# Optimization experiments

Hardware: AMD Instinct MI355X
Metric: run time of the kernel (lower is better)

The kernel has to match this reference:

```python
import jax, jax.numpy as jnp
import numpy as np
from math import ceil, log2

N_ROWS, M_COLS = 4096, 4096
LEVELS, FILT_LEN = 8, 16


def circ_conv(a, b, n):
    # circular convolution of each row of a with filter b, both zero-padded/truncated to length n
    return jnp.fft.irfft(jnp.fft.rfft(a, n=n) * jnp.fft.rfft(b, n=n), n=n)


def forward_level(x, w):
    # one forward DWT step over rows of x using wavelet filter w
    part = x.shape[1] // 2
    g = jnp.flip(w).at[1::2].multiply(-1.0)  # scaling filter g_k = (-1)^k h_{M-k-1}
    we, wo = w[::2], w[1::2]
    ge, go = g[::2], g[1::2]
    even, odd = x[:, ::2], x[:, 1::2]
    details = circ_conv(even, we, part) + circ_conv(odd, wo, part)
    approx = circ_conv(even, ge, part) + circ_conv(odd, go, part)
    return details, approx


def backward_level(details, approx, w):
    # one inverse DWT step: zero-upsample then circular-convolve with synthesis filters
    ws = jnp.flip(w)                       # wavelet synthesis
    ss = w.at[1::2].multiply(-1.0)         # scaling synthesis
    n, md = details.shape
    fd = jnp.zeros((n, 2 * md), details.dtype).at[:, ::2].set(details)
    fa = jnp.zeros((n, 2 * approx.shape[1]), approx.dtype).at[:, ::2].set(approx)
    return circ_conv(fd, ws, 2 * md) + circ_conv(fa, ss, 2 * approx.shape[1])


def despawn(x, wavelet):
    input_length = x.shape[1]
    target = 2 ** ceil(log2(input_length))
    x = jnp.pad(x, ((0, 0), (0, target - input_length)), mode='edge')  # ReplicationPad1d
    levels = wavelet.shape[0]
    approx = x
    coeffs = []
    for lvl in range(levels):
        d, approx = forward_level(approx, wavelet[lvl])
        coeffs.append(d)
    coeffs.append(approx)
    # inverse transform (note: original applies no thresholding in forward)
    rec = coeffs[-1]
    for lvl in reversed(range(levels)):
        rec = backward_level(coeffs[lvl], rec, wavelet[lvl])
    return rec[:, :input_length], jnp.concatenate(coeffs, axis=-1)


def setup_inputs() -> dict:
    key = jax.random.key(0)
    k1, k2 = jax.random.split(key)
    inp = jax.random.normal(k1, (N_ROWS, M_COLS), dtype=jnp.float32)
    wavelet = jax.random.normal(k2, (LEVELS, FILT_LEN), dtype=jnp.float32) * 0.3
    return {"input": inp, "wavelet": wavelet}


def reference(input, wavelet):
    return despawn(input, wavelet)
```

## Files before the change

kernel.cpp:

```cpp
#include <hip/hip_runtime.h>

#define NROWS 4096
#define NCOLS 4096
#define TPB   256


#define LD4(arr, base, vec) { float4 _v = (vec); (arr)[(base)] = _v.x; (arr)[(base)+1] = _v.y; (arr)[(base)+2] = _v.z; (arr)[(base)+3] = _v.w; }
#define LD2(arr, base, vec) { float2 _v = (vec); (arr)[(base)] = _v.x; (arr)[(base)+1] = _v.y; }

__device__ __forceinline__ void fwd_pt(const float* e8, const float* o8,
                                       const float* wl, float& dd, float& aa)
{
    float d = 0.f, a = 0.f;
    #pragma unroll
    for (int t = 0; t < 8; ++t) {
        float e = e8[-t], o = o8[-t];
        d = fmaf(wl[2*t],     e, d);
        d = fmaf(wl[2*t+1],   o, d);
        a = fmaf(wl[15-2*t],  e, a);
        a = fmaf(-wl[14-2*t], o, a);
    }
    dd = d; aa = a;
}

__device__ __forceinline__ void fwd_pt2(const float* e8, const float* o8,
                                        const float* wl, float& dd, float& aa)
{
    float d = 0.f, a = 0.f;
    #pragma unroll
    for (int t = 0; t < 8; ++t) {
        float e = e8[-2*t], o = o8[-2*t];
        d = fmaf(wl[2*t],     e, d);
        d = fmaf(wl[2*t+1],   o, d);
        a = fmaf(wl[15-2*t],  e, a);
        a = fmaf(-wl[14-2*t], o, a);
    }
    dd = d; aa = a;
}

__device__ __forceinline__ void bwd_pt(const float* d8, const float* a8,
                                       const float* wl, float& rr0, float& rr1)
{
    float x = 0.f, y = 0.f;
    #pragma unroll
    for (int t = 0; t < 8; ++t) {
        float dv = d8[-t], av = a8[-t];
        x = fmaf(wl[15-2*t], dv, x);
        x = fmaf(wl[2*t],    av, x);
        y = fmaf(wl[14-2*t], dv, y);
        y = fmaf(-wl[2*t+1], av, y);
    }
    rr0 = x; rr1 = y;
}

__global__ __launch_bounds__(TPB, 5) void despawn_kernel(
    const float* __restrict__ in, const float* __restrict__ wv,
    float* __restrict__ out_rec, float* __restrict__ out_coef)
{
    __shared__ float P0[2048];
    __shared__ float P1[1024];
    __shared__ float Csm[512];
    __shared__ float D0[2048];
    __shared__ float D1[1024];
    __shared__ float D2[512];

    const int tid = threadIdx.x;
    const int row = blockIdx.x;
    const float* rowIn = in + (size_t)row * NCOLS;
    float* crow = out_coef + (size_t)row * NCOLS;
    float* rrow = out_rec  + (size_t)row * NCOLS;

    float wl[16];

    {
        #pragma unroll
        for (int q = 0; q < 16; ++q) wl[q] = wv[q];
        const float4* X4 = (const float4*)rowIn;
        float xw[32];
        #pragma unroll
        for (int j = 0; j < 8; ++j) LD4(xw, 4*j, X4[(4*tid - 4 + j) & 1023]);
        float d[8], a[8];
        #pragma unroll
        for (int p = 0; p < 8; ++p) fwd_pt2(&xw[16 + 2*p], &xw[17 + 2*p], wl, d[p], a[p]);
        const int k0 = tid * 8;
        float4 d0v = make_float4(d[0], d[1], d[2], d[3]);
        float4 d1v = make_float4(d[4], d[5], d[6], d[7]);
        ((float4*)(crow + k0))[0] = d0v;
        ((float4*)(crow + k0))[1] = d1v;
        ((float4*)(D0 + k0))[0]   = d0v;
        ((float4*)(D0 + k0))[1]   = d1v;
        *(float4*)(P0 + (k0 >> 1))        = make_float4(a[0], a[2], a[4], a[6]);
        *(float4*)(P0 + 1024 + (k0 >> 1)) = make_float4(a[1], a[3], a[5], a[7]);
    }
    __syncthreads();

    {
        #pragma unroll
        for (int q = 0; q < 16; ++q) wl[q] = wv[16 + q];
        const float4* E4 = (const float4*)P0;
        const float4* O4 = (const float4*)(P0 + 1024);
        float xe[12], xo[12];
        #pragma unroll
        for (int j = 0; j < 3; ++j) {
            int idx = (tid - 2 + j) & 255;
            LD4(xe, 4*j, E4[idx]); LD4(xo, 4*j, O4[idx]);
        }
        float d[4], a[4];
        #pragma unroll
        for (int p = 0; p < 4; ++p) fwd_pt(&xe[8 + p], &xo[8 + p], wl, d[p], a[p]);
        const int k0 = tid * 4;
        float4 dv = make_float4(d[0], d[1], d[2], d[3]);
        *(float4*)(crow + 2048 + k0) = dv;
        *(float4*)(D1 + k0)          = dv;
        *(float2*)(P1 + (k0 >> 1))       = make_float2(a[0], a[2]);
        *(float2*)(P1 + 512 + (k0 >> 1)) = make_float2(a[1], a[3]);
    }
    __syncthreads();

    {
        #pragma unroll
        for (int q = 0; q < 16; ++q) wl[q] = wv[32 + q];
        const float2* Ev = (const float2*)P1;
        const float2* Ov = (const float2*)(P1 + 512);
        float xe[10], xo[10];
        #pragma unroll
        for (int j = 0; j < 5; ++j) {
            int idx = (tid - 4 + j) & 255;
            LD2(xe, 2*j, Ev[idx]); LD2(xo, 2*j, Ov[idx]);
        }
        float d[2], a[2];
        #pragma unroll
        for (int p = 0; p < 2; ++p) fwd_pt(&xe[8 + p], &xo[8 + p], wl, d[p], a[p]);
        const int k0 = tid * 2;
        float2 dv = make_float2(d[0], d[1]);
        *(float2*)(crow + 3072 + k0) = dv;
        *(float2*)(D2 + k0)          = dv;
        P0[tid]       = a[0];
        P0[256 + tid] = a[1];
    }
    __syncthreads();

    {
        const float* Ein = P0;
        float* aout = P0 + 512;
        int part = 256, cs = 0, cg = 3584;
        for (int lvl = 3; lvl < 8; ++lvl) {
            #pragma unroll
            for (int q = 0; q < 16; ++q) wl[q] = wv[16*lvl + q];
            const int nth = part >> 2;
            if (tid < nth) {
                const int pm = nth - 1;
                const float4* E4 = (const float4*)Ein;
                const float4* O4 = (const float4*)(Ein + part);
                float xe[12], xo[12];
                #pragma unroll
                for (int j = 0; j < 3; ++j) {
                    int idx = (tid - 2 + j) & pm;
                    LD4(xe, 4*j, E4[idx]); LD4(xo, 4*j, O4[idx]);
                }
                float d[4], a[4];
                #pragma unroll
                for (int p = 0; p < 4; ++p) fwd_pt(&xe[8 + p], &xo[8 + p], wl, d[p], a[p]);
                const int k0 = tid * 4;
                float4 dv = make_float4(d[0], d[1], d[2], d[3]);
                *(float4*)(Csm + cs + k0)  = dv;
                *(float4*)(crow + cg + k0) = dv;
                if (lvl == 7) {
                    float4 av = make_float4(a[0], a[1], a[2], a[3]);
                    *(float4*)(Csm + 496 + k0)   = av;
                    *(float4*)(crow + 4080 + k0) = av;
                } else {
                    *(float2*)(aout + (k0 >> 1))               = make_float2(a[0], a[2]);
                    *(float2*)(aout + (part >> 1) + (k0 >> 1)) = make_float2(a[1], a[3]);
                }
            }
            __syncthreads();
            Ein = aout; aout += part; cs += part; cg += part; part >>= 1;
        }
    }

    const float* A = Csm + 496;
    {
        float* outp = P0 + 1024;
        int md = 16, dOff = 480;
        for (int lvl = 7; lvl >= 3; --lvl) {
            #pragma unroll
            for (int q = 0; q < 16; ++q) wl[q] = wv[16*lvl + q];
            const int nth = md >> 2;
            if (tid < nth) {
                const int pm = nth - 1;
                const float4* D4 = (const float4*)(Csm + dOff);
                const float4* A4 = (const float4*)A;
                float xd[12], xa[12];
                #pragma unroll
                for (int j = 0; j < 3; ++j) {
                    int idx = (tid - 2 + j) & pm;
                    LD4(xd, 4*j, D4[idx]); LD4(xa, 4*j, A4[idx]);
                }
                float r0[4], r1[4];
                #pragma unroll
                for (int p = 0; p < 4; ++p) bwd_pt(&xd[8 + p], &xa[8 + p], wl, r0[p], r1[p]);
                const int j0 = tid * 4;
                ((float4*)(outp + 2*j0))[0] = make_float4(r0[0], r1[0], r0[1], r1[1]);
                ((float4*)(outp + 2*j0))[1] = make_float4(r0[2], r1[2], r0[3], r1[3]);
            }
            __syncthreads();
            A = outp; outp += 2*md; md <<= 1; dOff -= md;
        }
    }

    {
        #pragma unroll
        for (int q = 0; q < 16; ++q) wl[q] = wv[32 + q];
        const float2* Dg = (const float2*)D2;
        const float2* Av = (const float2*)(P0 + 1504);
        float xd[10], xa[10];
        #pragma unroll
        for (int j = 0; j < 5; ++j) {
            int idx = (tid - 4 + j) & 255;
            LD2(xd, 2*j, Dg[idx]); LD2(xa, 2*j, Av[idx]);
        }
        float r0[2], r1[2];
        #pragma unroll
        for (int p = 0; p < 2; ++p) bwd_pt(&xd[8 + p], &xa[8 + p], wl, r0[p], r1[p]);
        const int j0 = tid * 2;
        *(float4*)(P1 + 2*j0) = make_float4(r0[0], r1[0], r0[1], r1[1]);
    }
    __syncthreads();

    {
        #pragma unroll
        for (int q = 0; q < 16; ++q) wl[q] = wv[16 + q];
        const float4* Dg = (const float4*)D1;
        const float4* Av = (const float4*)P1;
        float xd[12], xa[12];
        #pragma unroll
        for (int j = 0; j < 3; ++j) {
            int idx = (tid - 2 + j) & 255;
            LD4(xd, 4*j, Dg[idx]); LD4(xa, 4*j, Av[idx]);
        }
        float r0[4], r1[4];
        #pragma unroll
        for (int p = 0; p < 4; ++p) bwd_pt(&xd[8 + p], &xa[8 + p], wl, r0[p], r1[p]);
        const int j0 = tid * 4;
        ((float4*)(P0 + 2*j0))[0] = make_float4(r0[0], r1[0], r0[1], r1[1]);
        ((float4*)(P0 + 2*j0))[1] = make_float4(r0[2], r1[2], r0[3], r1[3]);
    }
    __syncthreads();

    {
        #pragma unroll
        for (int q = 0; q < 16; ++q) wl[q] = wv[q];
        const float4* Dg = (const float4*)D0;
        const float4* Av = (const float4*)P0;
        const int j0 = tid * 8;
        {
            float xd[12], xa[12];
            #pragma unroll
            for (int c = 0; c < 3; ++c) {
                int idx = (2*tid - 2 + c) & 511;
                LD4(xd, 4*c, Dg[idx]); LD4(xa, 4*c, Av[idx]);
            }
            float r0[4], r1[4];
            #pragma unroll
            for (int p = 0; p < 4; ++p) bwd_pt(&xd[8 + p], &xa[8 + p], wl, r0[p], r1[p]);
            ((float4*)(rrow + 2*j0))[0] = make_float4(r0[0], r1[0], r0[1], r1[1]);
            ((float4*)(rrow + 2*j0))[1] = make_float4(r0[2], r1[2], r0[3], r1[3]);
        }
        {
            float xd[12], xa[12];
            #pragma unroll
            for (int c = 0; c < 3; ++c) {
                int idx = (2*tid - 1 + c) & 511;
                LD4(xd, 4*c, Dg[idx]); LD4(xa, 4*c, Av[idx]);
            }
            float r0[4], r1[4];
            #pragma unroll
            for (int p = 0; p < 4; ++p) bwd_pt(&xd[8 + p], &xa[8 + p], wl, r0[p], r1[p]);
            ((float4*)(rrow + 2*j0))[2] = make_float4(r0[0], r1[0], r0[1], r1[1]);
            ((float4*)(rrow + 2*j0))[3] = make_float4(r0[2], r1[2], r0[3], r1[3]);
        }
    }
}

extern "C" void kernel_launch(void* const* d_in, const int* in_sizes, int n_in,
                              void* d_out, int out_size, void* d_ws, size_t ws_size,
                              hipStream_t stream) {
    (void)in_sizes; (void)n_in; (void)d_ws; (void)ws_size; (void)out_size;
    const float* in = (const float*)d_in[0];
    const float* wv = (const float*)d_in[1];
    float* out_rec  = (float*)d_out;
    float* out_coef = (float*)d_out + (size_t)NROWS * NCOLS;
    despawn_kernel<<<NROWS, TPB, 0, stream>>>(in, wv, out_rec, out_coef);
}
```

Before: 56.53 us.

## Drop LDS detail buffers, reread details from global, split inverse outputs even/odd

Removes the shared-memory copies of the level 0-2 detail coefficients and has the inverse stages reread them from the just-written global coefficient output, which is expected to hit in cache. Inverse reconstructions are stored as separate even/odd halves, and a templated bwd_split reads them. This roughly halves LDS use so launch bounds can rise from 5 to 7 blocks per CU. The final stage is merged into one 8-point pass. The cost is global reads that depend on earlier global writes from the same block, plus possible register pressure under the tighter launch bound.

```diff
diff --git a/kernel.cpp b/kernel.cpp
--- a/kernel.cpp
+++ b/kernel.cpp
@@ -38,31 +38,35 @@
     dd = d; aa = a;
 }
 
-__device__ __forceinline__ void bwd_pt(const float* d8, const float* a8,
-                                       const float* wl, float& rr0, float& rr1)
-{
-    float x = 0.f, y = 0.f;
+template<int NP>
+__device__ __forceinline__ void bwd_split(const float* xd, const float* ae, const float* ao,
+                                          const float* wl, float* r0, float* r1)
+{
     #pragma unroll
-    for (int t = 0; t < 8; ++t) {
-        float dv = d8[-t], av = a8[-t];
-        x = fmaf(wl[15-2*t], dv, x);
-        x = fmaf(wl[2*t],    av, x);
-        y = fmaf(wl[14-2*t], dv, y);
-        y = fmaf(-wl[2*t+1], av, y);
-    }
-    rr0 = x; rr1 = y;
-}
-
-__global__ __launch_bounds__(TPB, 5) void despawn_kernel(
+    for (int p = 0; p < NP; ++p) {
+        float x = 0.f, y = 0.f;
+        #pragma unroll
+        for (int s = 0; s < 8; ++s) {
+            float dv = xd[8 + p - s];
+            const int m = p - s + 8;
+            float av = (m & 1) ? ao[(m - 1) >> 1] : ae[m >> 1];
+            x = fmaf(wl[15-2*s], dv, x);
+            x = fmaf(wl[2*s],    av, x);
+            y = fmaf(wl[14-2*s], dv, y);
+            y = fmaf(-wl[2*s+1], av, y);
+        }
+        r0[p] = x; r1[p] = y;
+    }
+}
+
+__global__ __launch_bounds__(TPB, 7) void despawn_kernel(
     const float* __restrict__ in, const float* __restrict__ wv,
     float* __restrict__ out_rec, float* __restrict__ out_coef)
 {
-    __shared__ float P0[2048];
-    __shared__ float P1[1024];
+    __shared__ float W0[2048];
+    __shared__ float W1[1024];
+    __shared__ float U[992];
     __shared__ float Csm[512];
-    __shared__ float D0[2048];
-    __shared__ float D1[1024];
-    __shared__ float D2[512];
 
     const int tid = threadIdx.x;
     const int row = blockIdx.x;
@@ -83,22 +87,18 @@
         #pragma unroll
         for (int p = 0; p < 8; ++p) fwd_pt2(&xw[16 + 2*p], &xw[17 + 2*p], wl, d[p], a[p]);
         const int k0 = tid * 8;
-        float4 d0v = make_float4(d[0], d[1], d[2], d[3]);
-        float4 d1v = make_float4(d[4], d[5], d[6], d[7]);
-        ((float4*)(crow + k0))[0] = d0v;
-        ((float4*)(crow + k0))[1] = d1v;
-        ((float4*)(D0 + k0))[0]   = d0v;
-        ((float4*)(D0 + k0))[1]   = d1v;
-        *(float4*)(P0 + (k0 >> 1))        = make_float4(a[0], a[2], a[4], a[6]);
-        *(float4*)(P0 + 1024 + (k0 >> 1)) = make_float4(a[1], a[3], a[5], a[7]);
+        ((float4*)(crow + k0))[0] = make_float4(d[0], d[1], d[2], d[3]);
+        ((float4*)(crow + k0))[1] = make_float4(d[4], d[5], d[6], d[7]);
+        *(float4*)(W0 + (k0 >> 1))        = make_float4(a[0], a[2], a[4], a[6]);
+        *(float4*)(W0 + 1024 + (k0 >> 1)) = make_float4(a[1], a[3], a[5], a[7]);
     }
     __syncthreads();
 
     {
         #pragma unroll
         for (int q = 0; q < 16; ++q) wl[q] = wv[16 + q];
-        const float4* E4 = (const float4*)P0;
-        const float4* O4 = (const float4*)(P0 + 1024);
+        const float4* E4 = (const float4*)W0;
+        const float4* O4 = (const float4*)(W0 + 1024);
         float xe[12], xo[12];
         #pragma unroll
         for (int j = 0; j < 3; ++j) {
@@ -109,19 +109,17 @@
         #pragma unroll
         for (int p = 0; p < 4; ++p) fwd_pt(&xe[8 + p], &xo[8 + p], wl, d[p], a[p]);
         const int k0 = tid * 4;
-        float4 dv = make_float4(d[0], d[1], d[2], d[3]);
-        *(float4*)(crow + 2048 + k0) = dv;
-        *(float4*)(D1 + k0)          = dv;
-        *(float2*)(P1 + (k0 >> 1))       = make_float2(a[0], a[2]);
-        *(float2*)(P1 + 512 + (k0 >> 1)) = make_float2(a[1], a[3]);
+        *(float4*)(crow + 2048 + k0) = make_float4(d[0], d[1], d[2], d[3]);
+        *(float2*)(W1 + (k0 >> 1))       = make_float2(a[0], a[2]);
+        *(float2*)(W1 + 512 + (k0 >> 1)) = make_float2(a[1], a[3]);
     }
     __syncthreads();
 
     {
         #pragma unroll
         for (int q = 0; q < 16; ++q) wl[q] = wv[32 + q];
-        const float2* Ev = (const float2*)P1;
-        const float2* Ov = (const float2*)(P1 + 512);
+        const float2* Ev = (const float2*)W1;
+        const float2* Ov = (const float2*)(W1 + 512);
         float xe[10], xo[10];
         #pragma unroll
         for (int j = 0; j < 5; ++j) {
@@ -132,17 +130,15 @@
         #pragma unroll
         for (int p = 0; p < 2; ++p) fwd_pt(&xe[8 + p], &xo[8 + p], wl, d[p], a[p]);
         const int k0 = tid * 2;
-        float2 dv = make_float2(d[0], d[1]);
-        *(float2*)(crow + 3072 + k0) = dv;
-        *(float2*)(D2 + k0)          = dv;
-        P0[tid]       = a[0];
-        P0[256 + tid] = a[1];
-    }
-    __syncthreads();
-
-    {
-        const float* Ein = P0;
-        float* aout = P0 + 512;
+        *(float2*)(crow + 3072 + k0) = make_float2(d[0], d[1]);
+        U[tid]       = a[0];
+        U[256 + tid] = a[1];
+    }
+    __syncthreads();
+
+    {
+        const float* Ein = U;
+        float* aout = U + 512;
         int part = 256, cs = 0, cg = 3584;
         for (int lvl = 3; lvl < 8; ++lvl) {
             #pragma unroll
@@ -166,9 +162,9 @@
                 *(float4*)(Csm + cs + k0)  = dv;
                 *(float4*)(crow + cg + k0) = dv;
                 if (lvl == 7) {
-                    float4 av = make_float4(a[0], a[1], a[2], a[3]);
-                    *(float4*)(Csm + 496 + k0)   = av;
-                    *(float4*)(crow + 4080 + k0) = av;
+                    *(float4*)(crow + 4080 + k0) = make_float4(a[0], a[1], a[2], a[3]);
+                    *(float2*)(Csm + 496 + 2*tid) = make_float2(a[0], a[2]);
+                    *(float2*)(Csm + 504 + 2*tid) = make_float2(a[1], a[3]);
                 } else {
                     *(float2*)(aout + (k0 >> 1))               = make_float2(a[0], a[2]);
                     *(float2*)(aout + (part >> 1) + (k0 >> 1)) = make_float2(a[1], a[3]);
@@ -179,9 +175,10 @@
         }
     }
 
-    const float* A = Csm + 496;
-    {
-        float* outp = P0 + 1024;
+    const float* AeP = Csm + 496;
+    const float* AoP = Csm + 504;
+    {
+        float* uout = U;
         int md = 16, dOff = 480;
         for (int lvl = 7; lvl >= 3; --lvl) {
             #pragma unroll
@@ -190,96 +187,90 @@
             if (tid < nth) {
                 const int pm = nth - 1;
                 const float4* D4 = (const float4*)(Csm + dOff);
-                const float4* A4 = (const float4*)A;
-                float xd[12], xa[12];
-                #pragma unroll
-                for (int j = 0; j < 3; ++j) {
-                    int idx = (tid - 2 + j) & pm;
-                    LD4(xd, 4*j, D4[idx]); LD4(xa, 4*j, A4[idx]);
+                float xd[12];
+                #pragma unroll
+                for (int j = 0; j < 3; ++j) LD4(xd, 4*j, D4[(tid - 2 + j) & pm]);
+                float ae[6], ao[6];
+                #pragma unroll
+                for (int c = 0; c < 3; ++c) {
+                    int idx = (tid - 2 + c) & pm;
+                    LD2(ae, 2*c, ((const float2*)AeP)[idx]);
+                    LD2(ao, 2*c, ((const float2*)AoP)[idx]);
                 }
                 float r0[4], r1[4];
-                #pragma unroll
-                for (int p = 0; p < 4; ++p) bwd_pt(&xd[8 + p], &xa[8 + p], wl, r0[p], r1[p]);
-                const int j0 = tid * 4;
-                ((float4*)(outp + 2*j0))[0] = make_float4(r0[0], r1[0], r0[1], r1[1]);
-                ((float4*)(outp + 2*j0))[1] = make_float4(r0[2], r1[2], r0[3], r1[3]);
+                bwd_split<4>(xd, ae, ao, wl, r0, r1);
+                *(float4*)(uout + 4*tid)      = make_float4(r0[0], r0[1], r0[2], r0[3]);
+                *(float4*)(uout + md + 4*tid) = make_float4(r1[0], r1[1], r1[2], r1[3]);
             }
             __syncthreads();
-            A = outp; outp += 2*md; md <<= 1; dOff -= md;
+            AeP = uout; AoP = uout + md;
+            uout += 2 * md; md <<= 1; dOff -= md;
         }
     }
 
     {
         #pragma unroll
         for (int q = 0; q < 16; ++q) wl[q] = wv[32 + q];
-        const float2* Dg = (const float2*)D2;
-        const float2* Av = (const float2*)(P0 + 1504);
-        float xd[10], xa[10];
-        #pragma unroll
-        for (int j = 0; j < 5; ++j) {
-            int idx = (tid - 4 + j) & 255;
-            LD2(xd, 2*j, Dg[idx]); LD2(xa, 2*j, Av[idx]);
+        const float2* Dg = (const float2*)(crow + 3072);
+        float xd[10];
+        #pragma unroll
+        for (int j = 0; j < 5; ++j) LD2(xd, 2*j, Dg[(tid - 4 + j) & 255]);
+        float ae[5], ao[5];
+        #pragma unroll
+        for (int q = 0; q < 5; ++q) {
+            int idx = (tid - 4 + q) & 255;
+            ae[q] = AeP[idx]; ao[q] = AoP[idx];
         }
         float r0[2], r1[2];
-        #pragma unroll
-        for (int p = 0; p < 2; ++p) bwd_pt(&xd[8 + p], &xa[8 + p], wl, r0[p], r1[p]);
-        const int j0 = tid * 2;
-        *(float4*)(P1 + 2*j0) = make_float4(r0[0], r1[0], r0[1], r1[1]);
+        bwd_split<2>(xd, ae, ao, wl, r0, r1);
+        *(float2*)(W1 + 2*tid)       = make_float2(r0[0], r0[1]);
+        *(float2*)(W1 + 512 + 2*tid) = make_float2(r1[0], r1[1]);
     }
     __syncthreads();
 
     {
         #pragma unroll
         for (int q = 0; q < 16; ++q) wl[q] = wv[16 + q];
-        const float4* Dg = (const float4*)D1;
-        const float4* Av = (const float4*)P1;
-        float xd[12], xa[12];
-        #pragma unroll
-        for (int j = 0; j < 3; ++j) {
-            int idx = (tid - 2 + j) & 255;
-            LD4(xd, 4*j, Dg[idx]); LD4(xa, 4*j, Av[idx]);
+        const float4* Dg = (const float4*)(crow + 2048);
+        float xd[12];
+        #pragma unroll
+        for (int j = 0; j < 3; ++j) LD4(xd, 4*j, Dg[(tid - 2 + j) & 255]);
+        float ae[6], ao[6];
+        #pragma unroll
+        for (int c = 0; c < 3; ++c) {
+            int idx = (tid - 2 + c) & 255;
+            LD2(ae, 2*c, ((const float2*)W1)[idx]);
+            LD2(ao, 2*c, ((const float2*)(W1 + 512))[idx]);
         }
         float r0[4], r1[4];
-        #pragma unroll
-        for (int p = 0; p < 4; ++p) bwd_pt(&xd[8 + p], &xa[8 + p], wl, r0[p], r1[p]);
-        const int j0 = tid * 4;
-        ((float4*)(P0 + 2*j0))[0] = make_float4(r0[0], r1[0], r0[1], r1[1]);
-        ((float4*)(P0 + 2*j0))[1] = make_float4(r0[2], r1[2], r0[3], r1[3]);
+        bwd_split<4>(xd, ae, ao, wl, r0, r1);
+        *(float4*)(W0 + 4*tid)        = make_float4(r0[0], r0[1], r0[2], r0[3]);
+        *(float4*)(W0 + 1024 + 4*tid) = make_float4(r1[0], r1[1], r1[2], r1[3]);
     }
     __syncthreads();
 
     {
         #pragma unroll
         for (int q = 0; q < 16; ++q) wl[q] = wv[q];
-        const float4* Dg = (const float4*)D0;
-        const float4* Av = (const float4*)P0;
+        const float4* Dg = (const float4*)crow;
+        float xd[16];
+        #pragma unroll
+        for (int c = 0; c < 4; ++c) LD4(xd, 4*c, Dg[(2*tid - 2 + c) & 511]);
+        float ae[8], ao[8];
+        #pragma unroll
+        for (int c = 0; c < 2; ++c) {
+            int idx = (tid - 1 + c) & 255;
+            LD4(ae, 4*c, ((const float4*)W0)[idx]);
+            LD4(ao, 4*c, ((const float4*)(W0 + 1024))[idx]);
+        }
+        float r0[8], r1[8];
+        bwd_split<8>(xd, ae, ao, wl, r0, r1);
         const int j0 = tid * 8;
-        {
-            float xd[12], xa[12];
-            #pragma unroll
-            for (int c = 0; c < 3; ++c) {
-                int idx = (2*tid - 2 + c) & 511;
-                LD4(xd, 4*c, Dg[idx]); LD4(xa, 4*c, Av[idx]);
-            }
-            float r0[4], r1[4];
-            #pragma unroll
-            for (int p = 0; p < 4; ++p) bwd_pt(&xd[8 + p], &xa[8 + p], wl, r0[p], r1[p]);
-            ((float4*)(rrow + 2*j0))[0] = make_float4(r0[0], r1[0], r0[1], r1[1]);
-            ((float4*)(rrow + 2*j0))[1] = make_float4(r0[2], r1[2], r0[3], r1[3]);
-        }
-        {
-            float xd[12], xa[12];
-            #pragma unroll
-            for (int c = 0; c < 3; ++c) {
-                int idx = (2*tid - 1 + c) & 511;
-                LD4(xd, 4*c, Dg[idx]); LD4(xa, 4*c, Av[idx]);
-            }
-            float r0[4], r1[4];
-            #pragma unroll
-            for (int p = 0; p < 4; ++p) bwd_pt(&xd[8 + p], &xa[8 + p], wl, r0[p], r1[p]);
-            ((float4*)(rrow + 2*j0))[2] = make_float4(r0[0], r1[0], r0[1], r1[1]);
-            ((float4*)(rrow + 2*j0))[3] = make_float4(r0[2], r1[2], r0[3], r1[3]);
-        }
+        float4* R = (float4*)(rrow + 2*j0);
+        R[0] = make_float4(r0[0], r1[0], r0[1], r1[1]);
+        R[1] = make_float4(r0[2], r1[2], r0[3], r1[3]);
+        R[2] = make_float4(r0[4], r1[4], r0[5], r1[5]);
+        R[3] = make_float4(r0[6], r1[6], r0[7], r1[7]);
     }
 }
 
```

Measured after the change: 55.75 us. About the same (-1.4%).

## Process two rows per block and read detail coefficients back from global

Applied to the files above, without the earlier changes.

Blocks now hold 512 threads and process two rows each, using per-row shared buffers. The shared D0/D1/D2 detail copies are removed, and the backward pass re-reads those coefficients from the just-written global output (crow) instead. This cuts shared memory per row so more rows can be resident on a CU. The cost is extra global reads that depend on same-block writes being visible after __syncthreads, plus larger blocks that synchronize two rows together.

```diff
diff --git a/kernel.cpp b/kernel.cpp
--- a/kernel.cpp
+++ b/kernel.cpp
@@ -2,7 +2,7 @@
 
 #define NROWS 4096
 #define NCOLS 4096
-#define TPB   256
+#define TPB   512
 
 
 #define LD4(arr, base, vec) { float4 _v = (vec); (arr)[(base)] = _v.x; (arr)[(base)+1] = _v.y; (arr)[(base)+2] = _v.z; (arr)[(base)+3] = _v.w; }
@@ -53,19 +53,22 @@
     rr0 = x; rr1 = y;
 }
 
-__global__ __launch_bounds__(TPB, 5) void despawn_kernel(
+__global__ __launch_bounds__(TPB, 8) void despawn_kernel(
     const float* __restrict__ in, const float* __restrict__ wv,
     float* __restrict__ out_rec, float* __restrict__ out_coef)
 {
-    __shared__ float P0[2048];
-    __shared__ float P1[1024];
-    __shared__ float Csm[512];
-    __shared__ float D0[2048];
-    __shared__ float D1[1024];
-    __shared__ float D2[512];
+    __shared__ float P0s[2][2048];
+    __shared__ float P1s[2][1024];
+    __shared__ float Csms[2][512];
 
     const int tid = threadIdx.x;
-    const int row = blockIdx.x;
+    const int r   = tid >> 8;
+    const int t   = tid & 255;
+    float* P0  = P0s[r];
+    float* P1  = P1s[r];
+    float* Csm = Csms[r];
+
+    const int row = blockIdx.x * 2 + r;
     const float* rowIn = in + (size_t)row * NCOLS;
     float* crow = out_coef + (size_t)row * NCOLS;
     float* rrow = out_rec  + (size_t)row * NCOLS;
@@ -78,17 +81,13 @@
         const float4* X4 = (const float4*)rowIn;
         float xw[32];
         #pragma unroll
-        for (int j = 0; j < 8; ++j) LD4(xw, 4*j, X4[(4*tid - 4 + j) & 1023]);
+        for (int j = 0; j < 8; ++j) LD4(xw, 4*j, X4[(4*t - 4 + j) & 1023]);
         float d[8], a[8];
         #pragma unroll
         for (int p = 0; p < 8; ++p) fwd_pt2(&xw[16 + 2*p], &xw[17 + 2*p], wl, d[p], a[p]);
-        const int k0 = tid * 8;
-        float4 d0v = make_float4(d[0], d[1], d[2], d[3]);
-        float4 d1v = make_float4(d[4], d[5], d[6], d[7]);
-        ((float4*)(crow + k0))[0] = d0v;
-        ((float4*)(crow + k0))[1] = d1v;
-        ((float4*)(D0 + k0))[0]   = d0v;
-        ((float4*)(D0 + k0))[1]   = d1v;
+        const int k0 = t * 8;
+        ((float4*)(crow + k0))[0] = make_float4(d[0], d[1], d[2], d[3]);
+        ((float4*)(crow + k0))[1] = make_float4(d[4], d[5], d[6], d[7]);
         *(float4*)(P0 + (k0 >> 1))        = make_float4(a[0], a[2], a[4], a[6]);
         *(float4*)(P0 + 1024 + (k0 >> 1)) = make_float4(a[1], a[3], a[5], a[7]);
     }
@@ -102,16 +101,14 @@
         float xe[12], xo[12];
         #pragma unroll
         for (int j = 0; j < 3; ++j) {
-            int idx = (tid - 2 + j) & 255;
+            int idx = (t - 2 + j) & 255;
             LD4(xe, 4*j, E4[idx]); LD4(xo, 4*j, O4[idx]);
         }
         float d[4], a[4];
         #pragma unroll
         for (int p = 0; p < 4; ++p) fwd_pt(&xe[8 + p], &xo[8 + p], wl, d[p], a[p]);
-        const int k0 = tid * 4;
-        float4 dv = make_float4(d[0], d[1], d[2], d[3]);
-        *(float4*)(crow + 2048 + k0) = dv;
-        *(float4*)(D1 + k0)          = dv;
+        const int k0 = t * 4;
+        *(float4*)(crow + 2048 + k0) = make_float4(d[0], d[1], d[2], d[3]);
         *(float2*)(P1 + (k0 >> 1))       = make_float2(a[0], a[2]);
         *(float2*)(P1 + 512 + (k0 >> 1)) = make_float2(a[1], a[3]);
     }
@@ -125,18 +122,16 @@
         float xe[10], xo[10];
         #pragma unroll
         for (int j = 0; j < 5; ++j) {
-            int idx = (tid - 4 + j) & 255;
+            int idx = (t - 4 + j) & 255;
             LD2(xe, 2*j, Ev[idx]); LD2(xo, 2*j, Ov[idx]);
         }
         float d[2], a[2];
         #pragma unroll
         for (int p = 0; p < 2; ++p) fwd_pt(&xe[8 + p], &xo[8 + p], wl, d[p], a[p]);
-        const int k0 = tid * 2;
-        float2 dv = make_float2(d[0], d[1]);
-        *(float2*)(crow + 3072 + k0) = dv;
-        *(float2*)(D2 + k0)          = dv;
-        P0[tid]       = a[0];
-        P0[256 + tid] = a[1];
+        const int k0 = t * 2;
+        *(float2*)(crow + 3072 + k0) = make_float2(d[0], d[1]);
+        P0[t]       = a[0];
+        P0[256 + t] = a[1];
     }
     __syncthreads();
 
@@ -148,20 +143,20 @@
             #pragma unroll
             for (int q = 0; q < 16; ++q) wl[q] = wv[16*lvl + q];
             const int nth = part >> 2;
-            if (tid < nth) {
+            if (t < nth) {
                 const int pm = nth - 1;
                 const float4* E4 = (const float4*)Ein;
                 const float4* O4 = (const float4*)(Ein + part);
                 float xe[12], xo[12];
                 #pragma unroll
                 for (int j = 0; j < 3; ++j) {
-                    int idx = (tid - 2 + j) & pm;
+                    int idx = (t - 2 + j) & pm;
                     LD4(xe, 4*j, E4[idx]); LD4(xo, 4*j, O4[idx]);
                 }
                 float d[4], a[4];
                 #pragma unroll
                 for (int p = 0; p < 4; ++p) fwd_pt(&xe[8 + p], &xo[8 + p], wl, d[p], a[p]);
-                const int k0 = tid * 4;
+                const int k0 = t * 4;
                 float4 dv = make_float4(d[0], d[1], d[2], d[3]);
                 *(float4*)(Csm + cs + k0)  = dv;
                 *(float4*)(crow + cg + k0) = dv;
@@ -187,20 +182,20 @@
             #pragma unroll
             for (int q = 0; q < 16; ++q) wl[q] = wv[16*lvl + q];
             const int nth = md >> 2;
-            if (tid < nth) {
+            if (t < nth) {
                 const int pm = nth - 1;
                 const float4* D4 = (const float4*)(Csm + dOff);
                 const float4* A4 = (const float4*)A;
                 float xd[12], xa[12];
                 #pragma unroll
                 for (int j = 0; j < 3; ++j) {
-                    int idx = (tid - 2 + j) & pm;
+                    int idx = (t - 2 + j) & pm;
                     LD4(xd, 4*j, D4[idx]); LD4(xa, 4*j, A4[idx]);
                 }
                 float r0[4], r1[4];
                 #pragma unroll
                 for (int p = 0; p < 4; ++p) bwd_pt(&xd[8 + p], &xa[8 + p], wl, r0[p], r1[p]);
-                const int j0 = tid * 4;
+                const int j0 = t * 4;
                 ((float4*)(outp + 2*j0))[0] = make_float4(r0[0], r1[0], r0[1], r1[1]);
                 ((float4*)(outp + 2*j0))[1] = make_float4(r0[2], r1[2], r0[3], r1[3]);
             }
@@ -212,18 +207,18 @@
     {
         #pragma unroll
         for (int q = 0; q < 16; ++q) wl[q] = wv[32 + q];
-        const float2* Dg = (const float2*)D2;
+        const float2* Dg = (const float2*)(crow + 3072);
         const float2* Av = (const float2*)(P0 + 1504);
         float xd[10], xa[10];
         #pragma unroll
         for (int j = 0; j < 5; ++j) {
-            int idx = (tid - 4 + j) & 255;
+            int idx = (t - 4 + j) & 255;
             LD2(xd, 2*j, Dg[idx]); LD2(xa, 2*j, Av[idx]);
         }
         float r0[2], r1[2];
         #pragma unroll
         for (int p = 0; p < 2; ++p) bwd_pt(&xd[8 + p], &xa[8 + p], wl, r0[p], r1[p]);
-        const int j0 = tid * 2;
+        const int j0 = t * 2;
         *(float4*)(P1 + 2*j0) = make_float4(r0[0], r1[0], r0[1], r1[1]);
     }
     __syncthreads();
@@ -231,18 +226,18 @@
     {
         #pragma unroll
         for (int q = 0; q < 16; ++q) wl[q] = wv[16 + q];
-        const float4* Dg = (const float4*)D1;
+        const float4* Dg = (const float4*)(crow + 2048);
         const float4* Av = (const float4*)P1;
         float xd[12], xa[12];
         #pragma unroll
         for (int j = 0; j < 3; ++j) {
-            int idx = (tid - 2 + j) & 255;
+            int idx = (t - 2 + j) & 255;
             LD4(xd, 4*j, Dg[idx]); LD4(xa, 4*j, Av[idx]);
         }
         float r0[4], r1[4];
         #pragma unroll
         for (int p = 0; p < 4; ++p) bwd_pt(&xd[8 + p], &xa[8 + p], wl, r0[p], r1[p]);
-        const int j0 = tid * 4;
+        const int j0 = t * 4;
         ((float4*)(P0 + 2*j0))[0] = make_float4(r0[0], r1[0], r0[1], r1[1]);
         ((float4*)(P0 + 2*j0))[1] = make_float4(r0[2], r1[2], r0[3], r1[3]);
     }
@@ -251,14 +246,14 @@
     {
         #pragma unroll
         for (int q = 0; q < 16; ++q) wl[q] = wv[q];
-        const float4* Dg = (const float4*)D0;
+        const float4* Dg = (const float4*)crow;
         const float4* Av = (const float4*)P0;
-        const int j0 = tid * 8;
+        const int j0 = t * 8;
         {
             float xd[12], xa[12];
             #pragma unroll
             for (int c = 0; c < 3; ++c) {
-                int idx = (2*tid - 2 + c) & 511;
+                int idx = (2*t - 2 + c) & 511;
                 LD4(xd, 4*c, Dg[idx]); LD4(xa, 4*c, Av[idx]);
             }
             float r0[4], r1[4];
@@ -271,7 +266,7 @@
             float xd[12], xa[12];
             #pragma unroll
             for (int c = 0; c < 3; ++c) {
-                int idx = (2*tid - 1 + c) & 511;
+                int idx = (2*t - 1 + c) & 511;
                 LD4(xd, 4*c, Dg[idx]); LD4(xa, 4*c, Av[idx]);
             }
             float r0[4], r1[4];
@@ -291,5 +286,5 @@
     const float* wv = (const float*)d_in[1];
     float* out_rec  = (float*)d_out;
     float* out_coef = (float*)d_out + (size_t)NROWS * NCOLS;
-    despawn_kernel<<<NROWS, TPB, 0, stream>>>(in, wv, out_rec, out_coef);
-}
+    despawn_kernel<<<NROWS / 2, TPB, 0, stream>>>(in, wv, out_rec, out_coef);
+}
```

After: 79.86 us. 1.41x slower.
